# Optimization experiments

Hardware: AMD Instinct MI355X
Metric: run time of the kernel (lower is better)

## Reference

```python
import jax, jax.numpy as jnp
import numpy as np

B, N, M, H, NH, IN, OUT = 64, 8192, 128, 512, 2, 128, 128
CTRL_IN = IN + NH * M  # 384


def setup_inputs() -> dict:
    key = jax.random.key(0)
    ks = jax.random.split(key, 20)
    d = {}
    d["x"] = jax.random.normal(ks[0], (B, IN), jnp.float32)
    d["prev_reads"] = jax.random.normal(ks[1], (NH, B, M), jnp.float32)
    d["h0"] = jax.random.normal(ks[2], (B, H), jnp.float32) * 0.1
    d["c0"] = jax.random.normal(ks[3], (B, H), jnp.float32) * 0.1
    wr = jax.random.uniform(ks[4], (NH, B, N), jnp.float32)
    ww = jax.random.uniform(ks[5], (NH, B, N), jnp.float32)
    d["prev_w_read"] = wr / jnp.sum(wr, axis=-1, keepdims=True)
    d["prev_w_write"] = ww / jnp.sum(ww, axis=-1, keepdims=True)
    d["memory"] = jax.random.normal(ks[6], (B, N, M), jnp.float32) * 0.1
    d["W_ih"] = jax.random.normal(ks[7], (4 * H, CTRL_IN), jnp.float32) * 0.02
    d["W_hh"] = jax.random.normal(ks[8], (4 * H, H), jnp.float32) * 0.02
    d["b_ih"] = jnp.zeros((4 * H,), jnp.float32)
    d["b_hh"] = jnp.zeros((4 * H,), jnp.float32)
    d["Wr"] = jax.random.normal(ks[9], (NH, M + 6, H), jnp.float32) * 0.05
    d["br"] = jnp.zeros((NH, M + 6), jnp.float32)
    d["Ww"] = jax.random.normal(ks[10], (NH, 3 * M + 6, H), jnp.float32) * 0.05
    d["bw"] = jnp.zeros((NH, 3 * M + 6), jnp.float32)
    d["fc_W"] = jax.random.normal(ks[11], (OUT, NH * M), jnp.float32) * 0.05
    d["fc_b"] = jnp.zeros((OUT,), jnp.float32)
    return d


def _lstm_cell(x, h, c, W_ih, W_hh, b_ih, b_hh):
    gates = x @ W_ih.T + b_ih + h @ W_hh.T + b_hh
    i, f, g, o = jnp.split(gates, 4, axis=1)  # torch gate order i,f,g,o
    i, f, o = jax.nn.sigmoid(i), jax.nn.sigmoid(f), jax.nn.sigmoid(o)
    c_new = f * c + i * jnp.tanh(g)
    return o * jnp.tanh(c_new), c_new


def _address(mem, k, beta, g, s, gamma, w_prev):
    # content addressing: cosine similarity (torch eps = 1e-8 on each norm)
    mem_e = mem + 1e-16
    k_e = k + 1e-16
    num = jnp.einsum('bnm,bm->bn', mem_e, k_e)
    den = jnp.maximum(jnp.linalg.norm(mem_e, axis=-1), 1e-8) * \
          jnp.maximum(jnp.linalg.norm(k_e, axis=-1), 1e-8)[:, None]
    wc = jax.nn.softmax(beta * num / den, axis=1)
    # interpolation
    wg = g * wc + (1.0 - g) * w_prev
    # circular convolution with 3-tap shift kernel s
    wt = s[:, 0:1] * jnp.roll(wg, 1, axis=1) + s[:, 1:2] * wg + s[:, 2:3] * jnp.roll(wg, -1, axis=1)
    # sharpening
    wp = wt ** gamma
    return wp / (jnp.sum(wp, axis=1, keepdims=True) + 1e-16)


def _split_params(o, m):
    k = o[:, :m]
    beta = jax.nn.softplus(o[:, m:m + 1])
    g = jax.nn.sigmoid(o[:, m + 1:m + 2])
    s = jax.nn.softmax(o[:, m + 2:m + 5], axis=1)
    gamma = 1.0 + jax.nn.softplus(o[:, m + 5:m + 6])
    return k, beta, g, s, gamma


def reference(x, prev_reads, h0, c0, prev_w_read, prev_w_write, memory,
              W_ih, W_hh, b_ih, b_hh, Wr, br, Ww, bw, fc_W, fc_b):
    nh, b, m = prev_reads.shape
    # controller input: [x, r_0, ..., r_{nh-1}]
    inp = jnp.concatenate([x, jnp.transpose(prev_reads, (1, 0, 2)).reshape(b, nh * m)], axis=1)
    ctrl_out, c_new = _lstm_cell(inp, h0, c0, W_ih, W_hh, b_ih, b_hh)
    reads = []
    mem = memory
    for i in range(nh):  # heads interleaved [read_i, write_i]; writes mutate memory
        # read head i
        ro = ctrl_out @ Wr[i].T + br[i]
        k, beta, g, s, gamma = _split_params(ro, m)
        w_r = _address(mem, k, beta, g, s, gamma, prev_w_read[i])
        reads.append(jnp.einsum('bn,bnm->bm', w_r, mem))
        # write head i
        wo = ctrl_out @ Ww[i].T + bw[i]
        k, beta, g, s, gamma = _split_params(wo, m)
        e = jax.nn.sigmoid(wo[:, m + 6:2 * m + 6])
        a = wo[:, 2 * m + 6:3 * m + 6]
        w_w = _address(mem, k, beta, g, s, gamma, prev_w_write[i])
        mem = mem * (1.0 - w_w[:, :, None] * e[:, None, :]) + w_w[:, :, None] * a[:, None, :]
    inp2 = jnp.concatenate(reads, axis=1)
    o = jax.nn.sigmoid(inp2 @ fc_W.T + fc_b)
    return o
```

## Files before the change

kernel.cpp:

```cpp
#include <hip/hip_runtime.h>

#define BB 64
#define NN 8192
#define MM 128
#define HH 512
#define KLSTM 896
#define JTOT 2048
#define COLS 658
#define OUTN 128
#define CHUNKS 32
#define PROW 388
#define RSTR 672

__device__ __forceinline__ float sigf(float x){ return 1.0f/(1.0f+__expf(-x)); }
__device__ __forceinline__ float tanhf_f(float x){ return 1.0f - 2.0f/(__expf(2.0f*x)+1.0f); }
__device__ __forceinline__ float softplusf_(float x){ return (x>20.0f)? x : log1pf(expf(x)); }

__global__ __launch_bounds__(128) void k_lstm_split(
    const float* __restrict__ x, const float* __restrict__ pr,
    const float* __restrict__ h0, const float* __restrict__ Wih,
    const float* __restrict__ Whh, float* __restrict__ GPART)
{
  __shared__ float a_s[64][68];
  __shared__ float w_s[64][36];
  int tid = threadIdx.x;
  int jt = blockIdx.x, ks = blockIdx.y;
  int jbase = jt*32;
  int cbeg = (ks<2)? ks*4 : 8 + (ks-2)*3;
  int cend = (ks<2)? cbeg+4 : cbeg+3;
  int jq = tid & 7, bq = tid >> 3;
  float4 acc0={0,0,0,0}, acc1={0,0,0,0}, acc2={0,0,0,0}, acc3={0,0,0,0};
  for (int c=cbeg; c<cend; ++c){
    int kc = c*64;
    __syncthreads();
    #pragma unroll
    for (int i=0;i<32;i++){
      int idx = tid + i*128;
      int kk = idx & 63, p = idx >> 6;
      int kg = kc + kk;
      float iv;
      if (kg < 128)      iv = x[p*128 + kg];
      else if (kg < 256) iv = pr[p*MM + (kg-128)];
      else if (kg < 384) iv = pr[BB*MM + p*MM + (kg-256)];
      else               iv = h0[p*HH + (kg-384)];
      a_s[kk][p] = iv;
    }
    #pragma unroll
    for (int i=0;i<16;i++){
      int idx = tid + i*128;
      int kk = idx & 63, j = idx >> 6;
      int kg = kc + kk;
      int jj = jbase + j;
      float wv = (kg < 384) ? Wih[(size_t)jj*384 + kg]
                            : Whh[(size_t)jj*512 + (kg-384)];
      w_s[kk][j] = wv;
    }
    __syncthreads();
    #pragma unroll 4
    for (int kk=0; kk<64; ++kk){
      float4 av = *(const float4*)&a_s[kk][bq*4];
      float4 wv = *(const float4*)&w_s[kk][jq*4];
      acc0.x += av.x*wv.x; acc0.y += av.x*wv.y; acc0.z += av.x*wv.z; acc0.w += av.x*wv.w;
      acc1.x += av.y*wv.x; acc1.y += av.y*wv.y; acc1.z += av.y*wv.z; acc1.w += av.y*wv.w;
      acc2.x += av.z*wv.x; acc2.y += av.z*wv.y; acc2.z += av.z*wv.z; acc2.w += av.z*wv.w;
      acc3.x += av.w*wv.x; acc3.y += av.w*wv.y; acc3.z += av.w*wv.z; acc3.w += av.w*wv.w;
    }
  }
  size_t base = (size_t)ks*BB*JTOT;
  int col = jbase + jq*4;
  *(float4*)&GPART[base + (size_t)(bq*4+0)*JTOT + col] = acc0;
  *(float4*)&GPART[base + (size_t)(bq*4+1)*JTOT + col] = acc1;
  *(float4*)&GPART[base + (size_t)(bq*4+2)*JTOT + col] = acc2;
  *(float4*)&GPART[base + (size_t)(bq*4+3)*JTOT + col] = acc3;
}

__global__ void k_ctrl(const float* __restrict__ GPART, const float* __restrict__ bih,
                       const float* __restrict__ bhh, const float* __restrict__ c0,
                       float* __restrict__ CTRL)
{
  int idx = blockIdx.x*256 + threadIdx.x;
  if (idx >= BB*HH) return;
  int b = idx >> 9, h = idx & 511;
  float g0 = bih[h]        + bhh[h];
  float g1 = bih[HH+h]     + bhh[HH+h];
  float g2 = bih[2*HH+h]   + bhh[2*HH+h];
  float g3 = bih[3*HH+h]   + bhh[3*HH+h];
  #pragma unroll
  for (int ks=0; ks<4; ++ks){
    const float* gp = GPART + ((size_t)ks*BB + b)*JTOT;
    g0 += gp[h]; g1 += gp[HH+h]; g2 += gp[2*HH+h]; g3 += gp[3*HH+h];
  }
  float i_ = sigf(g0), f_ = sigf(g1), gg = tanhf_f(g2), o_ = sigf(g3);
  CTRL[idx] = o_*tanhf_f(f_*c0[idx] + i_*gg);
}

__global__ __launch_bounds__(128) void k_head_split(
    const float* __restrict__ CTRL, const float* __restrict__ Wr,
    const float* __restrict__ Ww, float* __restrict__ RPART)
{
  __shared__ float c_s[64][68];
  __shared__ float w_s[64][36];
  int tid = threadIdx.x;
  int ct = blockIdx.x, ks = blockIdx.y;
  int cbase = ct*32;
  int jq = tid & 7, bq = tid >> 3;
  float4 acc0={0,0,0,0}, acc1={0,0,0,0}, acc2={0,0,0,0}, acc3={0,0,0,0};
  for (int cc=0; cc<2; ++cc){
    int kc = ks*128 + cc*64;
    __syncthreads();
    #pragma unroll
    for (int i=0;i<32;i++){
      int idx = tid + i*128;
      int kk = idx & 63, p = idx >> 6;
      c_s[kk][p] = CTRL[(size_t)p*HH + kc + kk];
    }
    #pragma unroll
    for (int i=0;i<16;i++){
      int idx = tid + i*128;
      int kk = idx & 63, j = idx >> 6;
      int col = cbase + j;
      int h = kc + kk;
      float wv = 0.0f;
      if (col < 134)       wv = Wr[(size_t)col*HH + h];
      else if (col < 524)  wv = Ww[(size_t)(col-134)*HH + h];
      else if (col < COLS) wv = Wr[(size_t)(134 + col-524)*HH + h];
      w_s[kk][j] = wv;
    }
    __syncthreads();
    #pragma unroll 4
    for (int kk=0; kk<64; ++kk){
      float4 av = *(const float4*)&c_s[kk][bq*4];
      float4 wv = *(const float4*)&w_s[kk][jq*4];
      acc0.x += av.x*wv.x; acc0.y += av.x*wv.y; acc0.z += av.x*wv.z; acc0.w += av.x*wv.w;
      acc1.x += av.y*wv.x; acc1.y += av.y*wv.y; acc1.z += av.y*wv.z; acc1.w += av.y*wv.w;
      acc2.x += av.z*wv.x; acc2.y += av.z*wv.y; acc2.z += av.z*wv.z; acc2.w += av.z*wv.w;
      acc3.x += av.w*wv.x; acc3.y += av.w*wv.y; acc3.z += av.w*wv.z; acc3.w += av.w*wv.w;
    }
  }
  size_t base = (size_t)ks*BB*RSTR;
  int col = cbase + jq*4;
  *(float4*)&RPART[base + (size_t)(bq*4+0)*RSTR + col] = acc0;
  *(float4*)&RPART[base + (size_t)(bq*4+1)*RSTR + col] = acc1;
  *(float4*)&RPART[base + (size_t)(bq*4+2)*RSTR + col] = acc2;
  *(float4*)&RPART[base + (size_t)(bq*4+3)*RSTR + col] = acc3;
}

__global__ __launch_bounds__(256) void k_params(
    const float* __restrict__ RPART, const float* __restrict__ br,
    const float* __restrict__ bw, float* __restrict__ COEF8,
    float* __restrict__ scal)
{
  int b = blockIdx.x, tid = threadIdx.x;
  __shared__ float ro[RSTR];
  __shared__ float wred[2][5];
  for (int idx=tid; idx<COLS; idx+=256){
    float s = (idx<134)? br[idx] : (idx<524)? bw[idx-134] : br[134 + idx-524];
    #pragma unroll
    for (int ks=0; ks<4; ++ks) s += RPART[((size_t)ks*BB + b)*RSTR + idx];
    ro[idx] = s;
  }
  __syncthreads();
  int m = tid & 127;
  float k0 = ro[m], kw = ro[134+m], k1 = ro[524+m];
  float e  = sigf(ro[268+m]);
  float a  = ro[396+m];
  if (tid < 128){
    float* c8 = COEF8 + ((size_t)b*MM + m)*8;
    *(float4*)c8     = make_float4(k0, kw, k1, e*k1);
    *(float4*)(c8+4) = make_float4(e, e*e, a, a*e);
  }
  float r0=k0*k0, r1=kw*kw, r2=k1*k1, r3=a*k1, r4=a*a;
  #pragma unroll
  for (int off=32; off; off>>=1){
    r0 += __shfl_xor(r0, off);
    r1 += __shfl_xor(r1, off);
    r2 += __shfl_xor(r2, off);
    r3 += __shfl_xor(r3, off);
    r4 += __shfl_xor(r4, off);
  }
  if (tid < 128 && (tid & 63) == 0){
    int w = tid >> 6;
    wred[w][0]=r0; wred[w][1]=r1; wred[w][2]=r2; wred[w][3]=r3; wred[w][4]=r4;
  }
  __syncthreads();
  if (tid < 3){
    float knsq = wred[0][tid] + wred[1][tid];
    float kn = fmaxf(sqrtf(knsq), 1e-8f);
    int base = (tid==0)? 0 : (tid==1)? 134 : 524;
    float beta  = softplusf_(ro[base+128]);
    float g     = sigf(ro[base+129]);
    float s0r = ro[base+130], s1r = ro[base+131], s2r = ro[base+132];
    float mx = fmaxf(s0r, fmaxf(s1r, s2r));
    float es0 = __expf(s0r-mx), es1 = __expf(s1r-mx), es2 = __expf(s2r-mx);
    float es = es0+es1+es2;
    float gamma = 1.0f + softplusf_(ro[base+133]);
    float* sc = scal + ((size_t)tid*BB + b)*8;
    sc[0]=beta; sc[1]=g; sc[2]=es0/es; sc[3]=es1/es; sc[4]=es2/es; sc[5]=gamma; sc[6]=kn;
  }
  if (tid == 3) scal[((size_t)3*BB + b)*8 + 0] = wred[0][3] + wred[1][3];
  if (tid == 4) scal[((size_t)3*BB + b)*8 + 1] = wred[0][4] + wred[1][4];
}

__global__ __launch_bounds__(256) void k_passA(
    const float* __restrict__ mem, const float* __restrict__ COEF8,
    float* __restrict__ OUT9)
{
  const size_t S = (size_t)BB*NN;
  int l = blockIdx.x;
  int xcd = l & 7, i = l >> 3;
  int b = xcd*8 + (i >> 5);
  int chunk = i & 31;
  int tid = threadIdx.x;
  __shared__ float vtile[32][257];
  const float4* cb = (const float4*)(COEF8 + (size_t)b*MM*8);
  int rowbase = chunk*256;
  float acc[9];
  #pragma unroll
  for (int q=0;q<9;q++) acc[q] = 0.f;
  for (int kc=0; kc<4; ++kc){
    __syncthreads();
    #pragma unroll
    for (int ii=0;ii<8;ii++){
      int f = tid + ii*256;
      int r = f >> 3, k4 = f & 7;
      float4 v = *(const float4*)(mem + ((size_t)b*NN + rowbase + r)*MM + kc*32 + k4*4);
      vtile[k4*4+0][r] = v.x;
      vtile[k4*4+1][r] = v.y;
      vtile[k4*4+2][r] = v.z;
      vtile[k4*4+3][r] = v.w;
    }
    __syncthreads();
    #pragma unroll
    for (int kk=0; kk<32; ++kk){
      int kg = kc*32 + kk;
      float4 cA = cb[kg*2];
      float4 cB = cb[kg*2+1];
      float v  = vtile[kk][tid];
      float vv = v*v;
      acc[0] += v*cA.x;  acc[1] += v*cA.y;  acc[2] += vv;
      acc[3] += v*cA.z;  acc[4] += v*cA.w;
      acc[5] += vv*cB.x; acc[6] += vv*cB.y;
      acc[7] += v*cB.z;  acc[8] += v*cB.w;
    }
  }
  size_t p = (size_t)b*NN + rowbase + tid;
  #pragma unroll
  for (int q=0;q<9;q++) OUT9[(size_t)q*S + p] = acc[q];
}

__global__ __launch_bounds__(512) void k_addr(
    const float* __restrict__ OUT9, const float* __restrict__ scal,
    const float* __restrict__ pwr, const float* __restrict__ pww,
    float* __restrict__ WR0 , float* __restrict__ WR1)
{
  const size_t S = (size_t)BB*NN;
  int l = blockIdx.x;
  int xcd = l & 7, j = l >> 3;
  int role = j >> 3;
  int b = xcd*8 + (j & 7);
  int tid = threadIdx.x;
  __shared__ float buf[NN];
  __shared__ float red[512];
  float wfin[16];

  {
    const float* numb = OUT9 + (size_t)role*S + (size_t)b*NN;
    const float* ssb  = OUT9 + 2*S + (size_t)b*NN;
    const float* wprev = ((role==0)? pwr : pww) + (size_t)b*NN;
    float* wo = WR0 + (size_t)role*S + (size_t)b*NN;
    const float* sc = scal + ((size_t)role*BB + b)*8;
    float beta=sc[0], g=sc[1], s0=sc[2], s1=sc[3], s2=sc[4], gamma=sc[5], kn=sc[6];
    float lmax = -1e30f;
    #pragma unroll
    for (int i=0;i<16;i++){
      int n = tid + i*512;
      float den = fmaxf(sqrtf(ssb[n]), 1e-8f) * kn;
      float lg = beta * numb[n] / den;
      buf[n] = lg;
      lmax = fmaxf(lmax, lg);
    }
    red[tid] = lmax; __syncthreads();
    for (int s=256; s>0; s>>=1){ if (tid<s) red[tid]=fmaxf(red[tid],red[tid+s]); __syncthreads(); }
    lmax = red[0]; __syncthreads();
    float lsum = 0.f;
    #pragma unroll
    for (int i=0;i<16;i++){ int n = tid + i*512; float e = __expf(buf[n]-lmax); buf[n]=e; lsum+=e; }
    red[tid] = lsum; __syncthreads();
    for (int s=256; s>0; s>>=1){ if (tid<s) red[tid]+=red[tid+s]; __syncthreads(); }
    float inv = 1.0f/red[0]; __syncthreads();
    #pragma unroll
    for (int i=0;i<16;i++){ int n = tid + i*512; float wc = buf[n]*inv; buf[n] = g*wc + (1.0f-g)*wprev[n]; }
    __syncthreads();
    float psum = 0.f;
    #pragma unroll
    for (int i=0;i<16;i++){
      int n = tid + i*512;
      float wm = buf[(n-1)&(NN-1)];
      float w0 = buf[n];
      float wp = buf[(n+1)&(NN-1)];
      float wt = s0*wm + s1*w0 + s2*wp;
      float p = __expf(gamma*__logf(wt));
      wfin[i] = p; psum += p;
    }
    red[tid] = psum; __syncthreads();
    for (int s=256; s>0; s>>=1){ if (tid<s) red[tid]+=red[tid+s]; __syncthreads(); }
    float invp = 1.0f/(red[0] + 1e-16f);
    #pragma unroll
    for (int i=0;i<16;i++){ wfin[i] *= invp; wo[tid + i*512] = wfin[i]; }
  }
  if (role == 0) return;

  __syncthreads();
  {
    const float* pb = OUT9 + (size_t)b*NN;
    const float* wp = pwr + S + (size_t)b*NN;
    float* wo = WR1 + (size_t)b*NN;
    const float* sc = scal + ((size_t)2*BB + b)*8;
    float beta=sc[0], g=sc[1], s0=sc[2], s1=sc[3], s2=sc[4], gamma=sc[5], kn=sc[6];
    const float* sc3 = scal + ((size_t)3*BB + b)*8;
    float akr1 = sc3[0], aa = sc3[1];
    float lmax = -1e30f;
    #pragma unroll
    for (int i=0;i<16;i++){
      int n = tid + i*512;
      float ss = pb[2*S+n], t3 = pb[3*S+n], t4 = pb[4*S+n];
      float t5 = pb[5*S+n], t6 = pb[6*S+n], t7 = pb[7*S+n], t8 = pb[8*S+n];
      float w = wfin[i];
      float num  = t3 + w*(akr1 - t4);
      float n1sq = ss + 2.0f*w*(t7 - t5) + w*w*(t6 + aa - 2.0f*t8);
      float nrm = sqrtf(fmaxf(n1sq, 0.f));
      float lg = beta * num / (fmaxf(nrm, 1e-8f) * kn);
      buf[n] = lg;
      lmax = fmaxf(lmax, lg);
    }
    red[tid] = lmax; __syncthreads();
    for (int s=256; s>0; s>>=1){ if (tid<s) red[tid]=fmaxf(red[tid],red[tid+s]); __syncthreads(); }
    lmax = red[0]; __syncthreads();
    float lsum = 0.f;
    #pragma unroll
    for (int i=0;i<16;i++){ int n = tid + i*512; float e = __expf(buf[n]-lmax); buf[n]=e; lsum+=e; }
    red[tid] = lsum; __syncthreads();
    for (int s=256; s>0; s>>=1){ if (tid<s) red[tid]+=red[tid+s]; __syncthreads(); }
    float inv = 1.0f/red[0]; __syncthreads();
    #pragma unroll
    for (int i=0;i<16;i++){ int n = tid + i*512; float wc = buf[n]*inv; buf[n] = g*wc + (1.0f-g)*wp[n]; }
    __syncthreads();
    float psum = 0.f;
    float wt_loc[16];
    #pragma unroll
    for (int i=0;i<16;i++){
      int n = tid + i*512;
      float wm = buf[(n-1)&(NN-1)];
      float w0 = buf[n];
      float wpv = buf[(n+1)&(NN-1)];
      float wt = s0*wm + s1*w0 + s2*wpv;
      float p = __expf(gamma*__logf(wt));
      wt_loc[i] = p; psum += p;
    }
    red[tid] = psum; __syncthreads();
    for (int s=256; s>0; s>>=1){ if (tid<s) red[tid]+=red[tid+s]; __syncthreads(); }
    float invp = 1.0f/(red[0] + 1e-16f);
    #pragma unroll
    for (int i=0;i<16;i++) wo[tid + i*512] = wt_loc[i]*invp;
  }
}

__global__ __launch_bounds__(256) void k_passF(
    const float* __restrict__ mem, const float* __restrict__ wr0,
    const float* __restrict__ wr1, const float* __restrict__ ww0,
    float* __restrict__ part)
{
  int l = blockIdx.x;
  int xcd = l & 7, i = l >> 3;
  int b = xcd*8 + (i >> 5);
  int chunk = i & 31;
  int tid = threadIdx.x, ty = tid>>5, lane = tid&31;
  float4 a0 = {0.f,0.f,0.f,0.f}, a1 = a0, a2 = a0;
  float w2 = 0.f;
  for (int it=0; it<32; ++it){
    int n = chunk*256 + it*8 + ty;
    size_t p = (size_t)b*NN + n;
    const float4* row = (const float4*)(mem + p*MM);
    float4 v = row[lane];
    float w0r = wr0[p], w1r = wr1[p], wwr = ww0[p];
    float w12 = w1r*wwr;
    a0.x += w0r*v.x; a0.y += w0r*v.y; a0.z += w0r*v.z; a0.w += w0r*v.w;
    a1.x += w1r*v.x; a1.y += w1r*v.y; a1.z += w1r*v.z; a1.w += w1r*v.w;
    a2.x += w12*v.x; a2.y += w12*v.y; a2.z += w12*v.z; a2.w += w12*v.w;
    if (lane==0) w2 += w12;
  }
  __shared__ float4 sred[256];
  __shared__ float w2s[8];
  float* prow = part + (size_t)(b*CHUNKS + chunk)*PROW;
  float4 accs[3] = {a0,a1,a2};
  #pragma unroll
  for (int q=0;q<3;q++){
    sred[tid] = accs[q];
    __syncthreads();
    if (ty == 0){
      float4 s = {0.f,0.f,0.f,0.f};
      #pragma unroll
      for (int r=0;r<8;r++){
        float4 t = sred[r*32 + lane];
        s.x += t.x; s.y += t.y; s.z += t.z; s.w += t.w;
      }
      ((float4*)(prow + q*MM))[lane] = s;
    }
    __syncthreads();
  }
  if (lane==0) w2s[ty] = w2;
  __syncthreads();
  if (tid==0){
    float s = 0.f;
    #pragma unroll
    for (int r=0;r<8;r++) s += w2s[r];
    prow[384] = s;
  }
}

__global__ __launch_bounds__(256) void k_tail(
    const float* __restrict__ part, const float* __restrict__ COEF8,
    const float* __restrict__ fcW, const float* __restrict__ fcb,
    float* __restrict__ out)
{
  int l = blockIdx.x;
  int b = (l & 7)*8 + (l >> 3);
  int tid = threadIdx.x;
  __shared__ float s_lds[384];
  __shared__ float inp2[256];
  __shared__ float w2sh;
  const float* pbase = part + (size_t)b*CHUNKS*PROW;
  for (int idx=tid; idx<384; idx+=256){
    float s = 0.f;
    for (int c=0;c<CHUNKS;c++) s += pbase[(size_t)c*PROW + idx];
    s_lds[idx] = s;
  }
  if (tid == 0){
    float w = 0.f;
    for (int c=0;c<CHUNKS;c++) w += pbase[(size_t)c*PROW + 384];
    w2sh = w;
  }
  __syncthreads();
  if (tid < 128){
    int m = tid;
    float e = COEF8[((size_t)b*MM + m)*8 + 4];
    float a = COEF8[((size_t)b*MM + m)*8 + 6];
    inp2[m] = s_lds[m];
    inp2[MM + m] = s_lds[MM + m] - e*s_lds[2*MM + m] + w2sh*a;
  }
  __syncthreads();
  if (tid < 128){
    int o = tid;
    float acc = fcb[o];
    const float4* wrow = (const float4*)(fcW + (size_t)o*(2*MM));
    const float4* i2 = (const float4*)inp2;
    #pragma unroll 8
    for (int k4=0; k4<64; ++k4){
      float4 w = wrow[k4];
      float4 v = i2[k4];
      acc += w.x*v.x + w.y*v.y + w.z*v.z + w.w*v.w;
    }
    out[(size_t)b*OUTN + o] = sigf(acc);
  }
}

extern "C" void kernel_launch(void* const* d_in, const int* in_sizes, int n_in,
                              void* d_out, int out_size, void* d_ws, size_t ws_size,
                              hipStream_t stream) {
  const float* x   = (const float*)d_in[0];
  const float* pr  = (const float*)d_in[1];
  const float* h0  = (const float*)d_in[2];
  const float* c0  = (const float*)d_in[3];
  const float* pwr = (const float*)d_in[4];
  const float* pww = (const float*)d_in[5];
  const float* mem = (const float*)d_in[6];
  const float* Wih = (const float*)d_in[7];
  const float* Whh = (const float*)d_in[8];
  const float* bih = (const float*)d_in[9];
  const float* bhh = (const float*)d_in[10];
  const float* Wr  = (const float*)d_in[11];
  const float* br  = (const float*)d_in[12];
  const float* Ww  = (const float*)d_in[13];
  const float* bw  = (const float*)d_in[14];
  const float* fcW = (const float*)d_in[15];
  const float* fcb = (const float*)d_in[16];
  float* out = (float*)d_out;

  float* ws = (float*)d_ws;
  size_t off = 0;
  auto alloc = [&](size_t n){ float* p = ws + off; off += n; return p; };
  const size_t S = (size_t)BB*NN;
  float* GPART = alloc((size_t)4*BB*JTOT);
  float* CTRL  = alloc((size_t)BB*HH);
  float* RPART = alloc((size_t)4*BB*RSTR);
  float* COEF8 = alloc((size_t)BB*MM*8);
  float* SCAL  = alloc((size_t)4*BB*8);
  float* OUT9  = alloc(9*S);
  float* WR0   = alloc(S);
  float* WW0   = alloc(S);
  float* WR1   = alloc(S);
  float* PART  = alloc((size_t)BB*CHUNKS*PROW);
  (void)ws_size; (void)in_sizes; (void)n_in; (void)out_size; (void)WW0;

  k_lstm_split<<<dim3(64,4), 128, 0, stream>>>(x, pr, h0, Wih, Whh, GPART);
  k_ctrl<<<(BB*HH+255)/256, 256, 0, stream>>>(GPART, bih, bhh, c0, CTRL);
  k_head_split<<<dim3(21,4), 128, 0, stream>>>(CTRL, Wr, Ww, RPART);
  k_params<<<BB, 256, 0, stream>>>(RPART, br, bw, COEF8, SCAL);
  k_passA<<<CHUNKS*BB, 256, 0, stream>>>(mem, COEF8, OUT9);
  k_addr<<<2*BB, 512, 0, stream>>>(OUT9, SCAL, pwr, pww, WR0, WR1);
  k_passF<<<CHUNKS*BB, 256, 0, stream>>>(mem, WR0, WR1, WW0, PART);
  k_tail<<<BB, 256, 0, stream>>>(PART, COEF8, fcW, fcb, out);
}
```

Baseline: 238.1 us.

## Cache bf16 copy of memory for second pass and fuse tail into passF

passA now writes a bf16 (round-to-nearest-even) copy of the memory tensor while it streams it, and passF reads that half-size copy instead of the fp32 memory. The intent is to halve the bytes passF reads, at the cost of extra writes in passA and reduced precision in the read vectors. The separate tail kernel is folded into passF through a per-batch atomic counter, so the last block for each batch does the final reduction and FC layer, removing one launch.

New measurement: 355.8 us. 1.49x slower.

```diff
diff --git a/kernel.cpp b/kernel.cpp
--- a/kernel.cpp
+++ b/kernel.cpp
@@ -15,15 +15,22 @@
 __device__ __forceinline__ float sigf(float x){ return 1.0f/(1.0f+__expf(-x)); }
 __device__ __forceinline__ float tanhf_f(float x){ return 1.0f - 2.0f/(__expf(2.0f*x)+1.0f); }
 __device__ __forceinline__ float softplusf_(float x){ return (x>20.0f)? x : log1pf(expf(x)); }
+__device__ __forceinline__ unsigned short bf16rne(float f){
+  unsigned int u = __float_as_uint(f);
+  u += 0x7FFFu + ((u >> 16) & 1u);
+  return (unsigned short)(u >> 16);
+}
 
 __global__ __launch_bounds__(128) void k_lstm_split(
     const float* __restrict__ x, const float* __restrict__ pr,
     const float* __restrict__ h0, const float* __restrict__ Wih,
-    const float* __restrict__ Whh, float* __restrict__ GPART)
-{
+    const float* __restrict__ Whh, float* __restrict__ GPART,
+    unsigned int* __restrict__ CNT)
+{
+  int tid = threadIdx.x;
+  if (blockIdx.x == 0 && blockIdx.y == 0 && tid < 64) CNT[tid] = 0;
   __shared__ float a_s[64][68];
   __shared__ float w_s[64][36];
-  int tid = threadIdx.x;
   int jt = blockIdx.x, ks = blockIdx.y;
   int jbase = jt*32;
   int cbeg = (ks<2)? ks*4 : 8 + (ks-2)*3;
@@ -203,7 +210,7 @@
 
 __global__ __launch_bounds__(256) void k_passA(
     const float* __restrict__ mem, const float* __restrict__ COEF8,
-    float* __restrict__ OUT9)
+    float* __restrict__ OUT9, unsigned short* __restrict__ MEMB)
 {
   const size_t S = (size_t)BB*NN;
   int l = blockIdx.x;
@@ -223,11 +230,15 @@
     for (int ii=0;ii<8;ii++){
       int f = tid + ii*256;
       int r = f >> 3, k4 = f & 7;
-      float4 v = *(const float4*)(mem + ((size_t)b*NN + rowbase + r)*MM + kc*32 + k4*4);
+      size_t eoff = ((size_t)b*NN + rowbase + r)*MM + kc*32 + k4*4;
+      float4 v = *(const float4*)(mem + eoff);
       vtile[k4*4+0][r] = v.x;
       vtile[k4*4+1][r] = v.y;
       vtile[k4*4+2][r] = v.z;
       vtile[k4*4+3][r] = v.w;
+      ushort4 h;
+      h.x = bf16rne(v.x); h.y = bf16rne(v.y); h.z = bf16rne(v.z); h.w = bf16rne(v.w);
+      *(ushort4*)(MEMB + eoff) = h;
     }
     __syncthreads();
     #pragma unroll
@@ -366,9 +377,11 @@
 }
 
 __global__ __launch_bounds__(256) void k_passF(
-    const float* __restrict__ mem, const float* __restrict__ wr0,
+    const unsigned short* __restrict__ memb, const float* __restrict__ wr0,
     const float* __restrict__ wr1, const float* __restrict__ ww0,
-    float* __restrict__ part)
+    const float* __restrict__ COEF8, const float* __restrict__ fcW,
+    const float* __restrict__ fcb, float* __restrict__ part,
+    unsigned int* __restrict__ CNT, float* __restrict__ out)
 {
   int l = blockIdx.x;
   int xcd = l & 7, i = l >> 3;
@@ -380,28 +393,33 @@
   for (int it=0; it<32; ++it){
     int n = chunk*256 + it*8 + ty;
     size_t p = (size_t)b*NN + n;
-    const float4* row = (const float4*)(mem + p*MM);
-    float4 v = row[lane];
+    const uint2* row = (const uint2*)(memb + p*MM);
+    uint2 u = row[lane];
+    float vx = __uint_as_float(u.x << 16);
+    float vy = __uint_as_float(u.x & 0xFFFF0000u);
+    float vz = __uint_as_float(u.y << 16);
+    float vw = __uint_as_float(u.y & 0xFFFF0000u);
     float w0r = wr0[p], w1r = wr1[p], wwr = ww0[p];
     float w12 = w1r*wwr;
-    a0.x += w0r*v.x; a0.y += w0r*v.y; a0.z += w0r*v.z; a0.w += w0r*v.w;
-    a1.x += w1r*v.x; a1.y += w1r*v.y; a1.z += w1r*v.z; a1.w += w1r*v.w;
-    a2.x += w12*v.x; a2.y += w12*v.y; a2.z += w12*v.z; a2.w += w12*v.w;
+    a0.x += w0r*vx; a0.y += w0r*vy; a0.z += w0r*vz; a0.w += w0r*vw;
+    a1.x += w1r*vx; a1.y += w1r*vy; a1.z += w1r*vz; a1.w += w1r*vw;
+    a2.x += w12*vx; a2.y += w12*vy; a2.z += w12*vz; a2.w += w12*vw;
     if (lane==0) w2 += w12;
   }
-  __shared__ float4 sred[256];
+  __shared__ float4 sred4[256];
   __shared__ float w2s[8];
+  __shared__ int lastFlag;
   float* prow = part + (size_t)(b*CHUNKS + chunk)*PROW;
   float4 accs[3] = {a0,a1,a2};
   #pragma unroll
   for (int q=0;q<3;q++){
-    sred[tid] = accs[q];
+    sred4[tid] = accs[q];
     __syncthreads();
     if (ty == 0){
       float4 s = {0.f,0.f,0.f,0.f};
       #pragma unroll
       for (int r=0;r<8;r++){
-        float4 t = sred[r*32 + lane];
+        float4 t = sred4[r*32 + lane];
         s.x += t.x; s.y += t.y; s.z += t.z; s.w += t.w;
       }
       ((float4*)(prow + q*MM))[lane] = s;
@@ -415,45 +433,42 @@
     #pragma unroll
     for (int r=0;r<8;r++) s += w2s[r];
     prow[384] = s;
-  }
-}
-
-__global__ __launch_bounds__(256) void k_tail(
-    const float* __restrict__ part, const float* __restrict__ COEF8,
-    const float* __restrict__ fcW, const float* __restrict__ fcb,
-    float* __restrict__ out)
-{
-  int l = blockIdx.x;
-  int b = (l & 7)*8 + (l >> 3);
-  int tid = threadIdx.x;
-  __shared__ float s_lds[384];
-  __shared__ float inp2[256];
-  __shared__ float w2sh;
+    __threadfence();
+    unsigned int old = atomicAdd(&CNT[b], 1u);
+    lastFlag = (old == CHUNKS-1);
+  }
+  __syncthreads();
+  if (!lastFlag) return;
+  __threadfence();
+
+  float* sraw = (float*)sred4;
   const float* pbase = part + (size_t)b*CHUNKS*PROW;
+  __syncthreads();
   for (int idx=tid; idx<384; idx+=256){
     float s = 0.f;
     for (int c=0;c<CHUNKS;c++) s += pbase[(size_t)c*PROW + idx];
-    s_lds[idx] = s;
+    sraw[idx] = s;
   }
   if (tid == 0){
     float w = 0.f;
     for (int c=0;c<CHUNKS;c++) w += pbase[(size_t)c*PROW + 384];
-    w2sh = w;
+    sraw[640] = w;
+    CNT[b] = 0;
   }
   __syncthreads();
   if (tid < 128){
     int m = tid;
     float e = COEF8[((size_t)b*MM + m)*8 + 4];
     float a = COEF8[((size_t)b*MM + m)*8 + 6];
-    inp2[m] = s_lds[m];
-    inp2[MM + m] = s_lds[MM + m] - e*s_lds[2*MM + m] + w2sh*a;
+    sraw[384 + m] = sraw[m];
+    sraw[384 + MM + m] = sraw[MM + m] - e*sraw[2*MM + m] + sraw[640]*a;
   }
   __syncthreads();
   if (tid < 128){
     int o = tid;
     float acc = fcb[o];
     const float4* wrow = (const float4*)(fcW + (size_t)o*(2*MM));
-    const float4* i2 = (const float4*)inp2;
+    const float4* i2 = (const float4*)(sraw + 384);
     #pragma unroll 8
     for (int k4=0; k4<64; ++k4){
       float4 w = wrow[k4];
@@ -500,14 +515,17 @@
   float* WW0   = alloc(S);
   float* WR1   = alloc(S);
   float* PART  = alloc((size_t)BB*CHUNKS*PROW);
+  float* CNTf  = alloc(64);
+  float* MEMBf = alloc(S*MM/2);
+  unsigned int* CNT = (unsigned int*)CNTf;
+  unsigned short* MEMB = (unsigned short*)MEMBf;
   (void)ws_size; (void)in_sizes; (void)n_in; (void)out_size; (void)WW0;
 
-  k_lstm_split<<<dim3(64,4), 128, 0, stream>>>(x, pr, h0, Wih, Whh, GPART);
+  k_lstm_split<<<dim3(64,4), 128, 0, stream>>>(x, pr, h0, Wih, Whh, GPART, CNT);
   k_ctrl<<<(BB*HH+255)/256, 256, 0, stream>>>(GPART, bih, bhh, c0, CTRL);
   k_head_split<<<dim3(21,4), 128, 0, stream>>>(CTRL, Wr, Ww, RPART);
   k_params<<<BB, 256, 0, stream>>>(RPART, br, bw, COEF8, SCAL);
-  k_passA<<<CHUNKS*BB, 256, 0, stream>>>(mem, COEF8, OUT9);
+  k_passA<<<CHUNKS*BB, 256, 0, stream>>>(mem, COEF8, OUT9, MEMB);
   k_addr<<<2*BB, 512, 0, stream>>>(OUT9, SCAL, pwr, pww, WR0, WR1);
-  k_passF<<<CHUNKS*BB, 256, 0, stream>>>(mem, WR0, WR1, WW0, PART);
-  k_tail<<<BB, 256, 0, stream>>>(PART, COEF8, fcW, fcb, out);
-}
+  k_passF<<<CHUNKS*BB, 256, 0, stream>>>(MEMB, WR0, WR1, WW0, COEF8, fcW, fcb, PART, CNT, out);
+}
```
